# Kernel optimization log

Measured on AMD Instinct MI355X. Metric: run time of the kernel, lower is better.

## Reference

```python
import jax, jax.numpy as jnp
import numpy as np

IN_CH = 512
OUT_CH = 512
NUM_GROUPS = 32
EPS = 1e-5


def setup_inputs() -> dict:
    key = jax.random.key(0)
    ks = jax.random.split(key, 8)
    N, C, H, W = 4, IN_CH, 64, 64
    s = 0.02
    return {
        "x": jax.random.normal(ks[0], (N, C, H, W), jnp.float32),
        "gn_scale": jnp.ones((C,), jnp.float32),
        "gn_bias": jnp.zeros((C,), jnp.float32),
        "wq": jax.random.normal(ks[1], (OUT_CH, C), jnp.float32) * s,
        "bq": jnp.zeros((OUT_CH,), jnp.float32),
        "wk": jax.random.normal(ks[2], (OUT_CH, C), jnp.float32) * s,
        "bk": jnp.zeros((OUT_CH,), jnp.float32),
        "wv": jax.random.normal(ks[3], (OUT_CH, C), jnp.float32) * s,
        "bv": jnp.zeros((OUT_CH,), jnp.float32),
        "wo": jax.random.normal(ks[4], (OUT_CH, OUT_CH), jnp.float32) * s,
        "bo": jnp.zeros((OUT_CH,), jnp.float32),
    }


def _group_norm(x, scale, bias):
    # x: [N, C, H, W] -> normalize per (group, spatial)
    N, C, H, W = x.shape
    g = x.reshape(N, NUM_GROUPS, C // NUM_GROUPS, H, W)
    mean = jnp.mean(g, axis=(2, 3, 4), keepdims=True)
    var = jnp.var(g, axis=(2, 3, 4), keepdims=True)
    g = (g - mean) * jax.lax.rsqrt(var + EPS)
    h = g.reshape(N, C, H, W)
    return h * scale[None, :, None, None] + bias[None, :, None, None]


def _conv1x1(x, w, b):
    # x: [N, C_in, H, W], w: [C_out, C_in] -> [N, C_out, H, W]
    return jnp.einsum('nchw,dc->ndhw', x, w) + b[None, :, None, None]


def reference(x, gn_scale, gn_bias, wq, bq, wk, bk, wv, bv, wo, bo):
    N, C, H, W = x.shape
    L = H * W
    h = _group_norm(x, gn_scale, gn_bias)
    q = _conv1x1(h, wq, bq).reshape(N, OUT_CH, L)
    k = _conv1x1(h, wk, bk).reshape(N, OUT_CH, L)
    v = _conv1x1(h, wv, bv).reshape(N, OUT_CH, L)
    scores = jnp.einsum('nci,ncj->nij', q, k) * (OUT_CH ** -0.5)  # [N, L, L]
    att = jax.nn.softmax(scores, axis=-1)
    out = jnp.einsum('nij,ncj->nci', att, v).reshape(N, OUT_CH, H, W)
    out = _conv1x1(out, wo, bo)
    return out + x  # skip_proj is Identity since in_ch == out_ch
```

## Files before the change

### kernel.cpp

```cpp
#include <hip/hip_runtime.h>
#include <math.h>

#define NB   4
#define CCH  512
#define LL   4096
#define GRP  32
#define CPG  16
#define CL   (CCH*LL)
#define EPSV 1e-5f

typedef __bf16 bf16x8 __attribute__((ext_vector_type(8)));
typedef float  f32x4  __attribute__((ext_vector_type(4)));

#define GLOAD_LDS16(g, l) __builtin_amdgcn_global_load_lds( \
    (const __attribute__((address_space(1))) void*)(g),     \
    (__attribute__((address_space(3))) void*)(l), 16, 0, 0)

__device__ __forceinline__ int swz_slot(int row, int q) {
    return 4 * row + (q ^ ((row >> 1) & 3));
}
__device__ __forceinline__ void swz_src(int l, int& jj, int& cc) {
    jj = l >> 2;
    cc = (l & 3) ^ ((l >> 3) & 3);
}

#define DPPF(x, ctrl) __builtin_bit_cast(float, \
    __builtin_amdgcn_update_dpp(0, __builtin_bit_cast(int, (x)), (ctrl), 0xf, 0xf, false))
__device__ __forceinline__ float red_sum16(float x) {
    x += DPPF(x, 0xB1); x += DPPF(x, 0x4E);
    x += DPPF(x, 0x124); x += DPPF(x, 0x128);
    return x;
}

__global__ __launch_bounds__(1024) void gn_stats(const float* __restrict__ x,
                                                 float* __restrict__ stats) {
    int n = blockIdx.x >> 5, g = blockIdx.x & 31;
    size_t base = ((size_t)n * CCH + (size_t)g * CPG) * LL;
    const float4* xp = (const float4*)(x + base);
    const int NV = CPG * LL / 4;
    int tid = threadIdx.x;
    float s1 = 0.f, s2 = 0.f;
    for (int i = tid; i < NV; i += 1024) {
        float4 v = xp[i];
        s1 += v.x + v.y + v.z + v.w;
        s2 += v.x*v.x + v.y*v.y + v.z*v.z + v.w*v.w;
    }
    __shared__ float red[32];
    for (int o = 32; o; o >>= 1) { s1 += __shfl_down(s1, o); s2 += __shfl_down(s2, o); }
    int lane = tid & 63, w = tid >> 6;
    if (!lane) { red[w] = s1; red[16 + w] = s2; }
    __syncthreads();
    if (tid == 0) {
        float a = 0.f, b = 0.f;
        for (int i = 0; i < 16; ++i) { a += red[i]; b += red[16 + i]; }
        const float inv_n = 1.f / (float)(CPG * LL);
        float mean = a * inv_n;
        float var  = b * inv_n - mean * mean;
        stats[blockIdx.x * 2]     = mean;
        stats[blockIdx.x * 2 + 1] = rsqrtf(var + EPSV);
    }
}

__global__ __launch_bounds__(256) void gn_norm_t(const float* __restrict__ x,
    const float* __restrict__ gamma, const float* __restrict__ beta,
    const float* __restrict__ stats, __bf16* __restrict__ Ht) {
    __shared__ float T[64][65];
    int n = blockIdx.z, c0 = blockIdx.y * 64, l0 = blockIdx.x * 64;
    int tid = threadIdx.x;
    int lx = tid & 63, py = tid >> 6;
    const float* xb = x + (size_t)n * CL;
#pragma unroll
    for (int p = 0; p < 16; ++p) {
        int cl = p * 4 + py;
        int c = c0 + cl;
        int g = c >> 4;
        float mean = stats[(n * GRP + g) * 2];
        float rstd = stats[(n * GRP + g) * 2 + 1];
        float sc = gamma[c] * rstd, bi = beta[c] - mean * sc;
        float v = xb[(size_t)c * LL + l0 + lx];
        T[lx][cl] = v * sc + bi;
    }
    __syncthreads();
    __bf16* hb = Ht + (size_t)n * CL;
#pragma unroll
    for (int p = 0; p < 16; ++p) {
        int ll = p * 4 + py;
        hb[(size_t)(l0 + ll) * CCH + c0 + lx] = (__bf16)T[ll][lx];
    }
}

__global__ __launch_bounds__(256) void tobf16(const float* __restrict__ src,
                                              __bf16* __restrict__ dst, int n) {
    int i = (blockIdx.x * 256 + threadIdx.x) * 4;
    if (i < n) {
        float4 v = *(const float4*)(src + i);
        dst[i]   = (__bf16)v.x; dst[i+1] = (__bf16)v.y;
        dst[i+2] = (__bf16)v.z; dst[i+3] = (__bf16)v.w;
    }
}

#define BM 128
#define BN 128
#define BK 32

template<int EPI>
__global__ __launch_bounds__(256) void gemm_nt(
    const __bf16* __restrict__ A, const __bf16* __restrict__ B,
    void* __restrict__ Cv, int M, int N, int K,
    long bsA, long bsB, long bsC, long bsR,
    const float* __restrict__ bias, const float* __restrict__ resid, float alpha)
{
    __shared__ __align__(16) __bf16 As[BM * BK];
    __shared__ __align__(16) __bf16 Bs[BN * BK];
    const int tid = threadIdx.x;
    const int l = tid & 63, w = tid >> 6;
    const int wm = w >> 1, wn = w & 1;
    const int m0 = blockIdx.y * BM, n0 = blockIdx.x * BN;
    A += (long)blockIdx.z * bsA;
    B += (long)blockIdx.z * bsB;

    f32x4 acc[4][4];
#pragma unroll
    for (int i = 0; i < 4; ++i)
#pragma unroll
        for (int j = 0; j < 4; ++j) acc[i][j] = f32x4{0.f, 0.f, 0.f, 0.f};

    int jj, cc; swz_src(l, jj, cc);
    const int slot = swz_slot(l & 15, l >> 4);

    const __bf16* Ag = A + (size_t)(m0 + w * 16 + jj) * K + cc * 8;
    const __bf16* Bg = B + (size_t)(n0 + w * 16 + jj) * K + cc * 8;
    char* AsB = (char*)As + w * 1024;
    char* BsB = (char*)Bs + w * 1024;

    for (int k0 = 0; k0 < K; k0 += BK) {
        GLOAD_LDS16(Ag + k0,                 AsB);
        GLOAD_LDS16(Ag + k0 + (size_t)64*K,  AsB + 4096);
        GLOAD_LDS16(Bg + k0,                 BsB);
        GLOAD_LDS16(Bg + k0 + (size_t)64*K,  BsB + 4096);
        __syncthreads();
        bf16x8 ar[4], br[4];
#pragma unroll
        for (int t = 0; t < 4; ++t) {
            ar[t] = *(const bf16x8*)(As + (wm*64 + t*16) * BK + slot * 8);
            br[t] = *(const bf16x8*)(Bs + (wn*64 + t*16) * BK + slot * 8);
        }
#pragma unroll
        for (int ti = 0; ti < 4; ++ti)
#pragma unroll
            for (int tj = 0; tj < 4; ++tj)
                acc[ti][tj] = __builtin_amdgcn_mfma_f32_16x16x32_bf16(
                    ar[ti], br[tj], acc[ti][tj], 0, 0, 0);
        __syncthreads();
    }

    const long cb = (long)blockIdx.z * bsC;
#pragma unroll
    for (int ti = 0; ti < 4; ++ti) {
#pragma unroll
        for (int r = 0; r < 4; ++r) {
            int m = m0 + wm*64 + ti*16 + (l >> 4)*4 + r;
            float bv = (EPI == 2 || EPI == 4) ? bias[m] : 0.f;
#pragma unroll
            for (int tj = 0; tj < 4; ++tj) {
                int n = n0 + wn*64 + tj*16 + (l & 15);
                float v = acc[ti][tj][r];
                if (EPI == 1) v += bias[n];
                if (EPI == 2 || EPI == 4) v += bv;
                if (EPI == 4) {
                    float rs = resid[(long)blockIdx.z * bsR + (size_t)m * N + n];
                    ((float*)Cv)[cb + (size_t)m * N + n] = v + rs;
                } else {
                    ((__bf16*)Cv)[cb + (size_t)m * N + n] = (__bf16)v;
                }
            }
        }
    }
}

#define PSTR 88

__global__ __launch_bounds__(512, 2) void flash_attn(
    const __bf16* __restrict__ Qt, const __bf16* __restrict__ Kt,
    const __bf16* __restrict__ Vb, __bf16* __restrict__ Ot)
{
    __shared__ __align__(16) __bf16 Ks[16 * 64 * 32];
    __shared__ __align__(16) __bf16 Vs[2 * 512 * 32];
    __shared__ float  Sm[64 * 68];
    __shared__ __align__(16) __bf16 Ps[64 * PSTR];
    __shared__ float lnv[64];

    const int tid = threadIdx.x;
    const int l = tid & 63, w = tid >> 6;
    const int wi = w & 3, kh = w >> 2;
    const int g = l >> 4, c = l & 15;
    const int b = (blockIdx.x & 7) >> 1;
    const int qt = ((blockIdx.x >> 3) << 1) | (blockIdx.x & 1);
    const int i0 = qt * 64;
    const size_t bb = (size_t)b * CL;
    const float alpha = 0.044194173824159216f;

    int jj, cc; swz_src(l, jj, cc);
    const int slot = swz_slot(c, g);

    bf16x8 Qf[8];
    {
        const __bf16* Qg = Qt + bb + (size_t)(i0 + wi*16 + c) * CCH + kh*256 + g*8;
#pragma unroll
        for (int kc = 0; kc < 8; ++kc) Qf[kc] = *(const bf16x8*)(Qg + kc * 32);
    }

    f32x4 Oacc[4][4];
#pragma unroll
    for (int mi = 0; mi < 4; ++mi)
#pragma unroll
        for (int ni = 0; ni < 4; ++ni) Oacc[mi][ni] = f32x4{0.f, 0.f, 0.f, 0.f};
    float l_r[4] = {0.f, 0.f, 0.f, 0.f};

    const __bf16* Kb = Kt + bb;
    const __bf16* Vg = Vb + bb;

    auto stageK = [&](int j0) {
#pragma unroll
        for (int q = 0; q < 2; ++q) {
            int kc = q * 8 + w;
#pragma unroll
            for (int p = 0; p < 4; ++p) {
                const __bf16* src = Kb + (size_t)(j0 + p*16 + jj) * CCH + kc*32 + cc*8;
                GLOAD_LDS16(src, (char*)Ks + kc*4096 + p*1024);
            }
        }
    };
    auto stageV = [&](int j0) {
#pragma unroll
        for (int jc = 0; jc < 2; ++jc)
#pragma unroll
            for (int p = 0; p < 4; ++p) {
                const __bf16* src = Vg + (size_t)(w*64 + p*16 + jj) * LL + j0 + jc*32 + cc*8;
                GLOAD_LDS16(src, (char*)Vs + jc*32768 + (w*64 + p*16)*64);
            }
    };

    stageK(0);
    for (int t = 0; t < 64; ++t) {
        __syncthreads();
        stageV(t * 64);

        f32x4 S[4];
#pragma unroll
        for (int tj = 0; tj < 4; ++tj) S[tj] = f32x4{0.f, 0.f, 0.f, 0.f};
#pragma unroll
        for (int kc = 0; kc < 8; ++kc) {
#pragma unroll
            for (int tj = 0; tj < 4; ++tj) {
                bf16x8 kf = *(const bf16x8*)(Ks + (kh*8 + kc)*2048 + tj*512 + slot*8);
                S[tj] = __builtin_amdgcn_mfma_f32_16x16x32_bf16(Qf[kc], kf, S[tj], 0, 0, 0);
            }
        }
        if (kh) {
#pragma unroll
            for (int tj = 0; tj < 4; ++tj)
#pragma unroll
                for (int r = 0; r < 4; ++r)
                    Sm[(wi*16 + g*4 + r)*68 + tj*16 + c] = S[tj][r];
        }
        __syncthreads();

        if (!kh) {
#pragma unroll
            for (int r = 0; r < 4; ++r) {
                int row = wi*16 + g*4 + r;
                float rs = 0.f;
#pragma unroll
                for (int tj = 0; tj < 4; ++tj) {
                    float p = __expf((S[tj][r] + Sm[row*68 + tj*16 + c]) * alpha);
                    rs += p;
                    Ps[row * PSTR + tj*16 + c] = (__bf16)p;
                }
                l_r[r] += rs;
            }
        } else {
            if (t < 63) stageK((t + 1) * 64);
        }
        __syncthreads();
        if (t < 63 && !kh) stageK((t + 1) * 64);

#pragma unroll
        for (int jc = 0; jc < 2; ++jc) {
            bf16x8 pa[4];
#pragma unroll
            for (int mi = 0; mi < 4; ++mi)
                pa[mi] = *(const bf16x8*)(Ps + (mi*16 + c) * PSTR + jc*32 + g*8);
#pragma unroll
            for (int ni = 0; ni < 4; ++ni) {
                bf16x8 vf = *(const bf16x8*)(Vs + jc*16384 + (w*64 + ni*16)*32 + slot*8);
#pragma unroll
                for (int mi = 0; mi < 4; ++mi)
                    Oacc[mi][ni] = __builtin_amdgcn_mfma_f32_16x16x32_bf16(pa[mi], vf, Oacc[mi][ni], 0, 0, 0);
            }
        }
    }

    if (!kh) {
#pragma unroll
        for (int r = 0; r < 4; ++r) {
            float tot = red_sum16(l_r[r]);
            if (c == 0) lnv[wi*16 + g*4 + r] = 1.f / tot;
        }
    }
    __syncthreads();
#pragma unroll
    for (int mi = 0; mi < 4; ++mi) {
#pragma unroll
        for (int r = 0; r < 4; ++r) {
            int row = mi*16 + g*4 + r;
            float inv = lnv[row];
#pragma unroll
            for (int ni = 0; ni < 4; ++ni) {
                int col = w*64 + ni*16 + c;
                Ot[bb + (size_t)(i0 + row) * CCH + col] = (__bf16)(Oacc[mi][ni][r] * inv);
            }
        }
    }
}

extern "C" void kernel_launch(void* const* d_in, const int* in_sizes, int n_in,
                              void* d_out, int out_size, void* d_ws, size_t ws_size,
                              hipStream_t stream) {
    const float* x   = (const float*)d_in[0];
    const float* gnw = (const float*)d_in[1];
    const float* gnb = (const float*)d_in[2];
    const float* wq  = (const float*)d_in[3];
    const float* bq  = (const float*)d_in[4];
    const float* wk  = (const float*)d_in[5];
    const float* bk  = (const float*)d_in[6];
    const float* wv  = (const float*)d_in[7];
    const float* bv  = (const float*)d_in[8];
    const float* wo  = (const float*)d_in[9];
    const float* bo  = (const float*)d_in[10];
    float* out = (float*)d_out;

    __bf16* wsb = (__bf16*)d_ws;
    const size_t NCL = (size_t)NB * CL;
    __bf16* Ht = wsb;
    __bf16* Qt = Ht + NCL;
    __bf16* Kt = Qt + NCL;
    __bf16* Vb = Kt + NCL;
    __bf16* Ot = Vb + NCL;
    __bf16* Wb = Ot + NCL;
    float* stats = (float*)(Wb + (size_t)4 * CCH * CCH);
    __bf16* wqb = Wb;
    __bf16* wkb = Wb + (size_t)CCH * CCH;
    __bf16* wvb = Wb + (size_t)2 * CCH * CCH;
    __bf16* wob = Wb + (size_t)3 * CCH * CCH;

    tobf16<<<256, 256, 0, stream>>>(wq, wqb, CCH * CCH);
    tobf16<<<256, 256, 0, stream>>>(wk, wkb, CCH * CCH);
    tobf16<<<256, 256, 0, stream>>>(wv, wvb, CCH * CCH);
    tobf16<<<256, 256, 0, stream>>>(wo, wob, CCH * CCH);

    gn_stats<<<NB * GRP, 1024, 0, stream>>>(x, stats);
    gn_norm_t<<<dim3(LL / 64, CCH / 64, NB), 256, 0, stream>>>(x, gnw, gnb, stats, Ht);

    gemm_nt<1><<<dim3(CCH / 128, LL / 128, NB), 256, 0, stream>>>(
        Ht, wqb, Qt, LL, CCH, CCH, CL, 0, CL, 0, bq, nullptr, 1.f);
    gemm_nt<1><<<dim3(CCH / 128, LL / 128, NB), 256, 0, stream>>>(
        Ht, wkb, Kt, LL, CCH, CCH, CL, 0, CL, 0, bk, nullptr, 1.f);
    gemm_nt<2><<<dim3(LL / 128, CCH / 128, NB), 256, 0, stream>>>(
        wvb, Ht, Vb, CCH, LL, CCH, 0, CL, CL, 0, bv, nullptr, 1.f);

    flash_attn<<<dim3(256), 512, 0, stream>>>(Qt, Kt, Vb, Ot);

    gemm_nt<4><<<dim3(LL / 128, CCH / 128, NB), 256, 0, stream>>>(
        wob, Ot, (void*)out, CCH, LL, CCH, 0, CL, CL, CL, bo, x, 1.f);
}
```

Baseline: 397.8 us.

## Fuse Q/K projections into one GEMM and re-tile flash-attention QK^T per wave

Merges the four weight-conversion launches into one 2D-grid kernel. Replaces the separate Q and K projection GEMMs with a single GEMM over concatenated weights, writing an interleaved QK buffer with row stride 1024. Re-tiles the score computation in flash attention so each wave computes a 32x32 block (two Q row tiles by two K column tiles) instead of 16x64, reusing each loaded K fragment across two MFMAs. Row sums are combined across the two column halves through shared memory. This reduces launch overhead and LDS traffic for K, at the cost of more registers for Q fragments and a strided QK layout.

```diff
diff --git a/kernel.cpp b/kernel.cpp
--- a/kernel.cpp
+++ b/kernel.cpp
@@ -8,6 +8,7 @@
 #define CPG  16
 #define CL   (CCH*LL)
 #define EPSV 1e-5f
+#define QSTR 1024
 
 typedef __bf16 bf16x8 __attribute__((ext_vector_type(8)));
 typedef float  f32x4  __attribute__((ext_vector_type(4)));
@@ -89,14 +90,16 @@
     }
 }
 
-__global__ __launch_bounds__(256) void tobf16(const float* __restrict__ src,
-                                              __bf16* __restrict__ dst, int n) {
+__global__ __launch_bounds__(256) void tobf16_4(
+    const float* __restrict__ s0, const float* __restrict__ s1,
+    const float* __restrict__ s2, const float* __restrict__ s3,
+    __bf16* __restrict__ dst) {
+    const float* sp = (blockIdx.y == 0) ? s0 : (blockIdx.y == 1) ? s1
+                    : (blockIdx.y == 2) ? s2 : s3;
     int i = (blockIdx.x * 256 + threadIdx.x) * 4;
-    if (i < n) {
-        float4 v = *(const float4*)(src + i);
-        dst[i]   = (__bf16)v.x; dst[i+1] = (__bf16)v.y;
-        dst[i+2] = (__bf16)v.z; dst[i+3] = (__bf16)v.w;
-    }
+    float4 v = *(const float4*)(sp + i);
+    __bf16* d = dst + (size_t)blockIdx.y * CCH * CCH + i;
+    d[0] = (__bf16)v.x; d[1] = (__bf16)v.y; d[2] = (__bf16)v.z; d[3] = (__bf16)v.w;
 }
 
 #define BM 128
@@ -108,7 +111,8 @@
     const __bf16* __restrict__ A, const __bf16* __restrict__ B,
     void* __restrict__ Cv, int M, int N, int K,
     long bsA, long bsB, long bsC, long bsR,
-    const float* __restrict__ bias, const float* __restrict__ resid, float alpha)
+    const float* __restrict__ bias, const float* __restrict__ bias2,
+    const float* __restrict__ resid)
 {
     __shared__ __align__(16) __bf16 As[BM * BK];
     __shared__ __align__(16) __bf16 Bs[BN * BK];
@@ -155,6 +159,7 @@
     }
 
     const long cb = (long)blockIdx.z * bsC;
+    const float* bn = (EPI == 5) ? ((n0 < 512) ? bias : (bias2 - 512)) : nullptr;
 #pragma unroll
     for (int ti = 0; ti < 4; ++ti) {
 #pragma unroll
@@ -165,7 +170,7 @@
             for (int tj = 0; tj < 4; ++tj) {
                 int n = n0 + wn*64 + tj*16 + (l & 15);
                 float v = acc[ti][tj][r];
-                if (EPI == 1) v += bias[n];
+                if (EPI == 5) v += bn[n];
                 if (EPI == 2 || EPI == 4) v += bv;
                 if (EPI == 4) {
                     float rs = resid[(long)blockIdx.z * bsR + (size_t)m * N + n];
@@ -181,33 +186,37 @@
 #define PSTR 88
 
 __global__ __launch_bounds__(512, 2) void flash_attn(
-    const __bf16* __restrict__ Qt, const __bf16* __restrict__ Kt,
-    const __bf16* __restrict__ Vb, __bf16* __restrict__ Ot)
+    const __bf16* __restrict__ QK, const __bf16* __restrict__ Vb,
+    __bf16* __restrict__ Ot)
 {
     __shared__ __align__(16) __bf16 Ks[16 * 64 * 32];
     __shared__ __align__(16) __bf16 Vs[2 * 512 * 32];
     __shared__ float  Sm[64 * 68];
     __shared__ __align__(16) __bf16 Ps[64 * PSTR];
-    __shared__ float lnv[64];
+    __shared__ float Lp[64 * 2];
 
     const int tid = threadIdx.x;
     const int l = tid & 63, w = tid >> 6;
-    const int wi = w & 3, kh = w >> 2;
+    const int wi = w & 1, jh = (w >> 1) & 1, kh = w >> 2;
     const int g = l >> 4, c = l & 15;
     const int b = (blockIdx.x & 7) >> 1;
     const int qt = ((blockIdx.x >> 3) << 1) | (blockIdx.x & 1);
     const int i0 = qt * 64;
-    const size_t bb = (size_t)b * CL;
+    const size_t bb2 = (size_t)b * LL * QSTR;
+    const size_t bb  = (size_t)b * CL;
     const float alpha = 0.044194173824159216f;
 
     int jj, cc; swz_src(l, jj, cc);
     const int slot = swz_slot(c, g);
 
-    bf16x8 Qf[8];
+    bf16x8 Qf[2][8];
     {
-        const __bf16* Qg = Qt + bb + (size_t)(i0 + wi*16 + c) * CCH + kh*256 + g*8;
-#pragma unroll
-        for (int kc = 0; kc < 8; ++kc) Qf[kc] = *(const bf16x8*)(Qg + kc * 32);
+        const __bf16* Qg = QK + bb2 + (size_t)(i0 + wi*32 + c) * QSTR + kh*256 + g*8;
+#pragma unroll
+        for (int mi = 0; mi < 2; ++mi)
+#pragma unroll
+            for (int kc = 0; kc < 8; ++kc)
+                Qf[mi][kc] = *(const bf16x8*)(Qg + (size_t)mi*16*QSTR + kc*32);
     }
 
     f32x4 Oacc[4][4];
@@ -215,9 +224,9 @@
     for (int mi = 0; mi < 4; ++mi)
 #pragma unroll
         for (int ni = 0; ni < 4; ++ni) Oacc[mi][ni] = f32x4{0.f, 0.f, 0.f, 0.f};
-    float l_r[4] = {0.f, 0.f, 0.f, 0.f};
-
-    const __bf16* Kb = Kt + bb;
+    float l_r[2][4] = {{0.f,0.f,0.f,0.f},{0.f,0.f,0.f,0.f}};
+
+    const __bf16* Kb = QK + bb2 + 512;
     const __bf16* Vg = Vb + bb;
 
     auto stageK = [&](int j0) {
@@ -226,7 +235,7 @@
             int kc = q * 8 + w;
 #pragma unroll
             for (int p = 0; p < 4; ++p) {
-                const __bf16* src = Kb + (size_t)(j0 + p*16 + jj) * CCH + kc*32 + cc*8;
+                const __bf16* src = Kb + (size_t)(j0 + p*16 + jj) * QSTR + kc*32 + cc*8;
                 GLOAD_LDS16(src, (char*)Ks + kc*4096 + p*1024);
             }
         }
@@ -246,38 +255,47 @@
         __syncthreads();
         stageV(t * 64);
 
-        f32x4 S[4];
-#pragma unroll
-        for (int tj = 0; tj < 4; ++tj) S[tj] = f32x4{0.f, 0.f, 0.f, 0.f};
+        f32x4 S[2][2];
+#pragma unroll
+        for (int mi = 0; mi < 2; ++mi)
+#pragma unroll
+            for (int tj = 0; tj < 2; ++tj) S[mi][tj] = f32x4{0.f,0.f,0.f,0.f};
 #pragma unroll
         for (int kc = 0; kc < 8; ++kc) {
 #pragma unroll
-            for (int tj = 0; tj < 4; ++tj) {
-                bf16x8 kf = *(const bf16x8*)(Ks + (kh*8 + kc)*2048 + tj*512 + slot*8);
-                S[tj] = __builtin_amdgcn_mfma_f32_16x16x32_bf16(Qf[kc], kf, S[tj], 0, 0, 0);
+            for (int tj = 0; tj < 2; ++tj) {
+                bf16x8 kf = *(const bf16x8*)(Ks + (kh*8 + kc)*2048 + (jh*2 + tj)*512 + slot*8);
+#pragma unroll
+                for (int mi = 0; mi < 2; ++mi)
+                    S[mi][tj] = __builtin_amdgcn_mfma_f32_16x16x32_bf16(Qf[mi][kc], kf, S[mi][tj], 0, 0, 0);
             }
         }
         if (kh) {
 #pragma unroll
-            for (int tj = 0; tj < 4; ++tj)
-#pragma unroll
-                for (int r = 0; r < 4; ++r)
-                    Sm[(wi*16 + g*4 + r)*68 + tj*16 + c] = S[tj][r];
+            for (int mi = 0; mi < 2; ++mi)
+#pragma unroll
+                for (int tj = 0; tj < 2; ++tj)
+#pragma unroll
+                    for (int r = 0; r < 4; ++r)
+                        Sm[(wi*32 + mi*16 + g*4 + r)*68 + (jh*2 + tj)*16 + c] = S[mi][tj][r];
         }
         __syncthreads();
 
         if (!kh) {
 #pragma unroll
-            for (int r = 0; r < 4; ++r) {
-                int row = wi*16 + g*4 + r;
-                float rs = 0.f;
-#pragma unroll
-                for (int tj = 0; tj < 4; ++tj) {
-                    float p = __expf((S[tj][r] + Sm[row*68 + tj*16 + c]) * alpha);
-                    rs += p;
-                    Ps[row * PSTR + tj*16 + c] = (__bf16)p;
+            for (int mi = 0; mi < 2; ++mi) {
+#pragma unroll
+                for (int r = 0; r < 4; ++r) {
+                    int row = wi*32 + mi*16 + g*4 + r;
+                    float rs = 0.f;
+#pragma unroll
+                    for (int tj = 0; tj < 2; ++tj) {
+                        float p = __expf((S[mi][tj][r] + Sm[row*68 + (jh*2 + tj)*16 + c]) * alpha);
+                        rs += p;
+                        Ps[row * PSTR + (jh*2 + tj)*16 + c] = (__bf16)p;
+                    }
+                    l_r[mi][r] += rs;
                 }
-                l_r[r] += rs;
             }
         } else {
             if (t < 63) stageK((t + 1) * 64);
@@ -303,10 +321,12 @@
 
     if (!kh) {
 #pragma unroll
-        for (int r = 0; r < 4; ++r) {
-            float tot = red_sum16(l_r[r]);
-            if (c == 0) lnv[wi*16 + g*4 + r] = 1.f / tot;
-        }
+        for (int mi = 0; mi < 2; ++mi)
+#pragma unroll
+            for (int r = 0; r < 4; ++r) {
+                float tot = red_sum16(l_r[mi][r]);
+                if (c == 0) Lp[(wi*32 + mi*16 + g*4 + r)*2 + jh] = tot;
+            }
     }
     __syncthreads();
 #pragma unroll
@@ -314,7 +334,7 @@
 #pragma unroll
         for (int r = 0; r < 4; ++r) {
             int row = mi*16 + g*4 + r;
-            float inv = lnv[row];
+            float inv = 1.f / (Lp[row*2] + Lp[row*2 + 1]);
 #pragma unroll
             for (int ni = 0; ni < 4; ++ni) {
                 int col = w*64 + ni*16 + c;
@@ -342,35 +362,27 @@
 
     __bf16* wsb = (__bf16*)d_ws;
     const size_t NCL = (size_t)NB * CL;
-    __bf16* Ht = wsb;
-    __bf16* Qt = Ht + NCL;
-    __bf16* Kt = Qt + NCL;
-    __bf16* Vb = Kt + NCL;
-    __bf16* Ot = Vb + NCL;
-    __bf16* Wb = Ot + NCL;
+    __bf16* Ht  = wsb;
+    __bf16* QKt = Ht + NCL;
+    __bf16* Vb  = QKt + 2 * NCL;
+    __bf16* Ot  = Vb + NCL;
+    __bf16* Wb  = Ot + NCL;
     float* stats = (float*)(Wb + (size_t)4 * CCH * CCH);
-    __bf16* wqb = Wb;
-    __bf16* wkb = Wb + (size_t)CCH * CCH;
-    __bf16* wvb = Wb + (size_t)2 * CCH * CCH;
-    __bf16* wob = Wb + (size_t)3 * CCH * CCH;
-
-    tobf16<<<256, 256, 0, stream>>>(wq, wqb, CCH * CCH);
-    tobf16<<<256, 256, 0, stream>>>(wk, wkb, CCH * CCH);
-    tobf16<<<256, 256, 0, stream>>>(wv, wvb, CCH * CCH);
-    tobf16<<<256, 256, 0, stream>>>(wo, wob, CCH * CCH);
-
+    __bf16* wqkb = Wb;
+    __bf16* wvb  = Wb + (size_t)2 * CCH * CCH;
+    __bf16* wob  = Wb + (size_t)3 * CCH * CCH;
+
+    tobf16_4<<<dim3(256, 4), 256, 0, stream>>>(wq, wk, wv, wo, Wb);
     gn_stats<<<NB * GRP, 1024, 0, stream>>>(x, stats);
     gn_norm_t<<<dim3(LL / 64, CCH / 64, NB), 256, 0, stream>>>(x, gnw, gnb, stats, Ht);
 
-    gemm_nt<1><<<dim3(CCH / 128, LL / 128, NB), 256, 0, stream>>>(
-        Ht, wqb, Qt, LL, CCH, CCH, CL, 0, CL, 0, bq, nullptr, 1.f);
-    gemm_nt<1><<<dim3(CCH / 128, LL / 128, NB), 256, 0, stream>>>(
-        Ht, wkb, Kt, LL, CCH, CCH, CL, 0, CL, 0, bk, nullptr, 1.f);
+    gemm_nt<5><<<dim3(1024 / 128, LL / 128, NB), 256, 0, stream>>>(
+        Ht, wqkb, QKt, LL, 1024, CCH, CL, 0, (long)LL * 1024, 0, bq, bk, nullptr);
     gemm_nt<2><<<dim3(LL / 128, CCH / 128, NB), 256, 0, stream>>>(
-        wvb, Ht, Vb, CCH, LL, CCH, 0, CL, CL, 0, bv, nullptr, 1.f);
-
-    flash_attn<<<dim3(256), 512, 0, stream>>>(Qt, Kt, Vb, Ot);
+        wvb, Ht, Vb, CCH, LL, CCH, 0, CL, CL, 0, bv, nullptr, nullptr);
+
+    flash_attn<<<dim3(256), 512, 0, stream>>>(QKt, Vb, Ot);
 
     gemm_nt<4><<<dim3(LL / 128, CCH / 128, NB), 256, 0, stream>>>(
-        wob, Ot, (void*)out, CCH, LL, CCH, 0, CL, CL, CL, bo, x, 1.f);
-}
+        wob, Ot, (void*)out, CCH, LL, CCH, 0, CL, CL, CL, bo, nullptr, x);
+}
```

Measured after the change: 391.4 us. Within noise of the previous version (-1.6%).
